# Optimization experiments

Measured on AMD Instinct MI355X. Metric: run time of the kernel, lower is better.

## Reference

```python
import jax, jax.numpy as jnp
import numpy as np

B, L, D_MODEL = 2, 1024, 512
D_INNER, D_STATE, DT_RANK, D_CONV = 1024, 16, 32, 4
N_LAYER, VOCAB, EMBED_DIM, NUM_EMOTIONS = 2, 30000, 256, 7


def setup_inputs() -> dict:
    key = jax.random.key(0)
    ks = jax.random.split(key, 12)
    def n(k, shape, scale=0.02):
        return jax.random.normal(k, shape, jnp.float32) * scale
    A_init = jnp.broadcast_to(jnp.arange(1, D_STATE + 1, dtype=jnp.float32), (N_LAYER, D_INNER, D_STATE))
    return {
        "input_ids": jax.random.randint(ks[0], (B, L), 0, VOCAB),
        "embedding": n(ks[1], (VOCAB, D_MODEL)),
        "norm_w": jnp.ones((N_LAYER, D_MODEL)),
        "in_proj_w": n(ks[2], (N_LAYER, D_MODEL, 2 * D_INNER)),
        "conv_w": n(ks[3], (N_LAYER, D_INNER, 1, D_CONV), 0.1),
        "conv_b": jnp.zeros((N_LAYER, D_INNER)),
        "x_proj_w": n(ks[4], (N_LAYER, D_INNER, DT_RANK + 2 * D_STATE)),
        "dt_proj_w": n(ks[5], (N_LAYER, DT_RANK, D_INNER), 0.1),
        "dt_proj_b": jnp.zeros((N_LAYER, D_INNER)),
        "A_log": jnp.log(A_init),
        "D": jnp.ones((N_LAYER, D_INNER)),
        "out_proj_w": n(ks[6], (N_LAYER, D_INNER, D_MODEL)),
        "norm_f_w": jnp.ones((D_MODEL,)),
        "proj_w": n(ks[7], (D_MODEL, EMBED_DIM)),
        "proj_b": jnp.zeros((EMBED_DIM,)),
        "cls_w": n(ks[8], (EMBED_DIM, NUM_EMOTIONS)),
        "cls_b": jnp.zeros((NUM_EMOTIONS,)),
    }


def rmsnorm(x, w, eps=1e-5):
    return x * jax.lax.rsqrt(jnp.mean(x * x, axis=-1, keepdims=True) + eps) * w


def selective_scan(u, delta, A, B_, C, D_):
    # u, delta: [b,l,d]; A: [d,n]; B_, C: [b,l,n]; D_: [d]
    dA = jnp.exp(jnp.einsum('bld,dn->bldn', delta, A))          # [b,l,d,n]
    dBu = jnp.einsum('bld,bln,bld->bldn', delta, B_, u)          # [b,l,d,n]
    def step(h, inp):
        dA_t, dBu_t, C_t = inp                                   # [b,d,n],[b,d,n],[b,n]
        h = dA_t * h + dBu_t
        y = jnp.einsum('bdn,bn->bd', h, C_t)
        return h, y
    h0 = jnp.zeros((u.shape[0], u.shape[2], A.shape[1]), u.dtype)
    _, ys = jax.lax.scan(step, h0, (dA.transpose(1, 0, 2, 3), dBu.transpose(1, 0, 2, 3), C.transpose(1, 0, 2)))
    return ys.transpose(1, 0, 2) + u * D_                        # [b,l,d]


def mamba_block(x, in_w, cw, cb, xp_w, dt_w, dt_b, A_log, D_, out_w):
    # x: [b,l,d_model]
    xr = x @ in_w                                                # [b,l,2*d_inner]
    xi, res = jnp.split(xr, 2, axis=-1)
    # causal depthwise conv1d over time
    xc = jax.lax.conv_general_dilated(
        xi.transpose(0, 2, 1), cw, window_strides=(1,),
        padding=[(D_CONV - 1, 0)], feature_group_count=D_INNER,
        dimension_numbers=('NCH', 'OIH', 'NCH'))
    xi = jax.nn.silu(xc.transpose(0, 2, 1) + cb)                 # [b,l,d_inner]
    x_dbl = xi @ xp_w
    delta, B_, C = jnp.split(x_dbl, [DT_RANK, DT_RANK + D_STATE], axis=-1)
    delta = jax.nn.softplus(delta @ dt_w + dt_b)                 # [b,l,d_inner]
    A = -jnp.exp(A_log)
    y = selective_scan(xi, delta, A, B_, C, D_)
    y = y * jax.nn.silu(res)
    return y @ out_w                                             # [b,l,d_model]


def reference(input_ids, embedding, norm_w, in_proj_w, conv_w, conv_b, x_proj_w,
              dt_proj_w, dt_proj_b, A_log, D, out_proj_w, norm_f_w,
              proj_w, proj_b, cls_w, cls_b):
    x = embedding[input_ids]                                     # [b,l,d_model]
    for i in range(N_LAYER):
        x = x + mamba_block(rmsnorm(x, norm_w[i]), in_proj_w[i], conv_w[i],
                            conv_b[i], x_proj_w[i], dt_proj_w[i], dt_proj_b[i],
                            A_log[i], D[i], out_proj_w[i])
    x = rmsnorm(x, norm_f_w)
    pooled = x.mean(axis=1)                                      # [b,d_model]
    emotion_emb = pooled @ proj_w + proj_b                       # [b,embed_dim]
    logits = emotion_emb @ cls_w + cls_b                         # [b,num_emotions]
    return logits, emotion_emb
```

## Files before the change

kernel.cpp:

```cpp
#include <hip/hip_runtime.h>
#include <cstddef>

#define D_MODEL   512
#define D_INNER   1024
#define D_STATE   16
#define DT_RANK   32
#define SEQ_L     1024
#define BATCH     2
#define NLAYER    2
#define M_ROWS    (BATCH * SEQ_L)
#define NC        64
#define LC        (SEQ_L / NC)

typedef __bf16 bf16x8 __attribute__((ext_vector_type(8)));
typedef float  f32x4  __attribute__((ext_vector_type(4)));

__device__ __forceinline__ float softplus_f(float x) {
    return fmaxf(x, 0.f) + log1pf(expf(-fabsf(x)));
}
__device__ __forceinline__ float silu_f(float x) {
    return x / (1.f + __expf(-x));
}
__device__ __forceinline__ unsigned short f2bf(float f) {
    unsigned u = __float_as_uint(f);
    return (unsigned short)((u + 0x7fffu + ((u >> 16) & 1u)) >> 16);
}
__device__ __forceinline__ float bf2f(unsigned short v) {
    return __uint_as_float(((unsigned)v) << 16);
}
__device__ __forceinline__ unsigned pack_bf2(float lo, float hi) {
    return (unsigned)f2bf(lo) | ((unsigned)f2bf(hi) << 16);
}

__global__ void embed_kernel(const int* __restrict__ ids,
                             const float* __restrict__ emb,
                             float* __restrict__ x) {
    int g = blockIdx.x * blockDim.x + threadIdx.x;
    int c = (g & 127) << 2;
    int m = g >> 7;
    int row = ids[m];
    *(float4*)&x[(size_t)m * D_MODEL + c] =
        *(const float4*)&emb[(size_t)row * D_MODEL + c];
}

__global__ __launch_bounds__(64) void rmsnorm_bf_kernel(const float* __restrict__ x,
                                                        const float* __restrict__ w,
                                                        unsigned short* __restrict__ out) {
    int row = blockIdx.x;
    int tid = threadIdx.x;
    const float* xp = x + (size_t)row * D_MODEL;
    float4 v0 = *(const float4*)&xp[tid * 4];
    float4 v1 = *(const float4*)&xp[256 + tid * 4];
    float ss = v0.x*v0.x + v0.y*v0.y + v0.z*v0.z + v0.w*v0.w
             + v1.x*v1.x + v1.y*v1.y + v1.z*v1.z + v1.w*v1.w;
    #pragma unroll
    for (int off = 32; off > 0; off >>= 1) ss += __shfl_xor(ss, off);
    float scale = rsqrtf(ss * (1.f / D_MODEL) + 1e-5f);
    float4 w0 = *(const float4*)&w[tid * 4];
    float4 w1 = *(const float4*)&w[256 + tid * 4];
    unsigned short* op = out + (size_t)row * D_MODEL;
    uint2 p0, p1;
    p0.x = pack_bf2(v0.x * scale * w0.x, v0.y * scale * w0.y);
    p0.y = pack_bf2(v0.z * scale * w0.z, v0.w * scale * w0.w);
    p1.x = pack_bf2(v1.x * scale * w1.x, v1.y * scale * w1.y);
    p1.y = pack_bf2(v1.z * scale * w1.z, v1.w * scale * w1.w);
    *(uint2*)&op[tid * 4] = p0;
    *(uint2*)&op[256 + tid * 4] = p1;
}

__global__ __launch_bounds__(256) void castT_kernel(const float* __restrict__ W,
                                                    unsigned short* __restrict__ Wt,
                                                    int K, int N) {
    W  += (size_t)blockIdx.z * K * N;
    Wt += (size_t)blockIdx.z * K * N;
    __shared__ float tile[32][33];
    int n0 = blockIdx.x * 32, k0 = blockIdx.y * 32;
    int tx = threadIdx.x & 31, ty = threadIdx.x >> 5;
    #pragma unroll
    for (int i = 0; i < 4; ++i)
        tile[ty + i*8][tx] = W[(size_t)(k0 + ty + i*8) * N + n0 + tx];
    __syncthreads();
    #pragma unroll
    for (int i = 0; i < 4; ++i)
        Wt[(size_t)(n0 + ty + i*8) * K + k0 + tx] = f2bf(tile[tx][ty + i*8]);
}

__global__ __launch_bounds__(256) void gemm_mfma128(const unsigned short* __restrict__ A,
                                                    const unsigned short* __restrict__ Bt,
                                                    unsigned short* __restrict__ Cb,
                                                    int K, int ldc) {
    __shared__ unsigned short As[128 * 64];
    __shared__ unsigned short Bs[128 * 64];
    int m0 = blockIdx.y * 128;
    int n0 = blockIdx.x * 128;
    int t = threadIdx.x;
    int lane = t & 63, wave = t >> 6;
    int wr = wave >> 1, wc = wave & 1;
    int srow = t >> 3;
    int sc8  = t & 7;
    f32x4 acc[4][4] = {};

    for (int k0 = 0; k0 < K; k0 += 64) {
        __syncthreads();
        #pragma unroll
        for (int i = 0; i < 4; ++i) {
            int row = i * 32 + srow;
            int csrc = sc8 ^ (row & 7);
            __builtin_amdgcn_global_load_lds(
                (const __attribute__((address_space(1))) void*)
                    &A[(size_t)(m0 + row) * K + k0 + csrc * 8],
                (__attribute__((address_space(3))) void*)
                    &As[row * 64 + sc8 * 8], 16, 0, 0);
            __builtin_amdgcn_global_load_lds(
                (const __attribute__((address_space(1))) void*)
                    &Bt[(size_t)(n0 + row) * K + k0 + csrc * 8],
                (__attribute__((address_space(3))) void*)
                    &Bs[row * 64 + sc8 * 8], 16, 0, 0);
        }
        __syncthreads();
        #pragma unroll
        for (int ks = 0; ks < 2; ++ks) {
            bf16x8 av[4], bv[4];
            #pragma unroll
            for (int f = 0; f < 4; ++f) {
                int ar = wr * 64 + f * 16 + (lane & 15);
                int ac = (ks * 4 + (lane >> 4)) ^ (ar & 7);
                av[f] = *reinterpret_cast<const bf16x8*>(&As[ar * 64 + ac * 8]);
                int br = wc * 64 + f * 16 + (lane & 15);
                int bc = (ks * 4 + (lane >> 4)) ^ (br & 7);
                bv[f] = *reinterpret_cast<const bf16x8*>(&Bs[br * 64 + bc * 8]);
            }
            #pragma unroll
            for (int fm = 0; fm < 4; ++fm)
                #pragma unroll
                for (int fn = 0; fn < 4; ++fn)
                    acc[fm][fn] = __builtin_amdgcn_mfma_f32_16x16x32_bf16(
                        av[fm], bv[fn], acc[fm][fn], 0, 0, 0);
        }
    }
    #pragma unroll
    for (int fm = 0; fm < 4; ++fm)
        #pragma unroll
        for (int fn = 0; fn < 4; ++fn) {
            int row = m0 + wr * 64 + fm * 16 + (lane >> 4) * 4;
            int col = n0 + wc * 64 + fn * 16 + (lane & 15);
            #pragma unroll
            for (int r = 0; r < 4; ++r)
                Cb[(size_t)(row + r) * ldc + col] = f2bf(acc[fm][fn][r]);
        }
}

__global__ __launch_bounds__(256) void gemm_mfma64_acc(const unsigned short* __restrict__ A,
                                                       const unsigned short* __restrict__ Bt,
                                                       float* __restrict__ C,
                                                       int K, int ldc) {
    __shared__ unsigned short As[64 * 64];
    __shared__ unsigned short Bs[64 * 64];
    int m0 = blockIdx.y * 64;
    int n0 = blockIdx.x * 64;
    int t = threadIdx.x;
    int lane = t & 63, wave = t >> 6;
    int wr = wave >> 1, wc = wave & 1;
    int srow = t >> 3;
    int sc8  = t & 7;
    f32x4 acc[2][2] = {};

    for (int k0 = 0; k0 < K; k0 += 64) {
        __syncthreads();
        #pragma unroll
        for (int i = 0; i < 2; ++i) {
            int row = i * 32 + srow;
            int csrc = sc8 ^ (row & 7);
            __builtin_amdgcn_global_load_lds(
                (const __attribute__((address_space(1))) void*)
                    &A[(size_t)(m0 + row) * K + k0 + csrc * 8],
                (__attribute__((address_space(3))) void*)
                    &As[row * 64 + sc8 * 8], 16, 0, 0);
            __builtin_amdgcn_global_load_lds(
                (const __attribute__((address_space(1))) void*)
                    &Bt[(size_t)(n0 + row) * K + k0 + csrc * 8],
                (__attribute__((address_space(3))) void*)
                    &Bs[row * 64 + sc8 * 8], 16, 0, 0);
        }
        __syncthreads();
        #pragma unroll
        for (int ks = 0; ks < 2; ++ks) {
            bf16x8 av[2], bv[2];
            #pragma unroll
            for (int f = 0; f < 2; ++f) {
                int ar = wr * 32 + f * 16 + (lane & 15);
                int ac = (ks * 4 + (lane >> 4)) ^ (ar & 7);
                av[f] = *reinterpret_cast<const bf16x8*>(&As[ar * 64 + ac * 8]);
                int br = wc * 32 + f * 16 + (lane & 15);
                int bc = (ks * 4 + (lane >> 4)) ^ (br & 7);
                bv[f] = *reinterpret_cast<const bf16x8*>(&Bs[br * 64 + bc * 8]);
            }
            #pragma unroll
            for (int fm = 0; fm < 2; ++fm)
                #pragma unroll
                for (int fn = 0; fn < 2; ++fn)
                    acc[fm][fn] = __builtin_amdgcn_mfma_f32_16x16x32_bf16(
                        av[fm], bv[fn], acc[fm][fn], 0, 0, 0);
        }
    }
    #pragma unroll
    for (int fm = 0; fm < 2; ++fm)
        #pragma unroll
        for (int fn = 0; fn < 2; ++fn) {
            int row = m0 + wr * 32 + fm * 16 + (lane >> 4) * 4;
            int col = n0 + wc * 32 + fn * 16 + (lane & 15);
            #pragma unroll
            for (int r = 0; r < 4; ++r)
                C[(size_t)(row + r) * ldc + col] += acc[fm][fn][r];
        }
}

__global__ void conv_bf_kernel(const unsigned short* __restrict__ xi,
                               const float* __restrict__ cw,
                               const float* __restrict__ cb,
                               unsigned short* __restrict__ u) {
    int g = blockIdx.x * blockDim.x + threadIdx.x;
    int d = g & (D_INNER - 1);
    int m = g >> 10;
    int l = m & (SEQ_L - 1);
    float4 w = *(const float4*)&cw[d * 4];
    const unsigned short* col = &xi[(size_t)m * 2048 + d];
    float x3 = bf2f(col[0]);
    float x2 = (l >= 1) ? bf2f(col[-2048]) : 0.f;
    float x1 = (l >= 2) ? bf2f(col[-4096]) : 0.f;
    float x0 = (l >= 3) ? bf2f(col[-6144]) : 0.f;
    u[g] = f2bf(silu_f(cb[d] + w.x*x0 + w.y*x1 + w.z*x2 + w.w*x3));
}

__global__ __launch_bounds__(256) void xproj_kernel(const unsigned short* __restrict__ u,
                                                    const float* __restrict__ Bw,
                                                    float* __restrict__ Cc) {
    __shared__ float Bsh[64][68];
    __shared__ float Ash[4][64];
    int row0 = blockIdx.x * 4;
    int t = threadIdx.x;
    int tr = t >> 6, c = t & 63;
    int kk = t >> 2, cb4 = (t & 3) << 4;
    float acc = 0.f;
    for (int k0 = 0; k0 < 1024; k0 += 64) {
        __syncthreads();
        #pragma unroll
        for (int j = 0; j < 4; ++j) {
            float4 v = *(const float4*)&Bw[(size_t)(k0 + kk) * 64 + cb4 + j * 4];
            *(float4*)&Bsh[kk][cb4 + j * 4] = v;
        }
        Ash[tr][c] = bf2f(u[(size_t)(row0 + tr) * 1024 + k0 + c]);
        __syncthreads();
        #pragma unroll
        for (int k = 0; k < 64; ++k)
            acc = fmaf(Ash[tr][k], Bsh[k][c], acc);
    }
    Cc[(size_t)(row0 + tr) * 64 + c] = acc;
}

__global__ __launch_bounds__(256) void scan_p1f(const unsigned short* __restrict__ u,
                                                const float* __restrict__ xdbl,
                                                const float* __restrict__ dtw,
                                                const float* __restrict__ dtb_,
                                                const float* __restrict__ A_log,
                                                float* __restrict__ aprod,
                                                float* __restrict__ hloc) {
    int tid = threadIdx.x;
    int d = blockIdx.x * 256 + tid;
    int b = blockIdx.y, c = blockIdx.z;
    int l0 = c * LC;
    __shared__ float sX[LC][64];
    __shared__ float sW[32][256];
    #pragma unroll
    for (int k = 0; k < 32; ++k)
        sW[k][tid] = dtw[k * 1024 + blockIdx.x * 256 + tid];
    for (int i = tid; i < LC * 64; i += 256) {
        int l = i >> 6, j = i & 63;
        sX[l][j] = xdbl[(size_t)(b * SEQ_L + l0 + l) * 64 + j];
    }
    __syncthreads();
    float A_[D_STATE], h[D_STATE], ap[D_STATE];
    #pragma unroll
    for (int n = 0; n < D_STATE; ++n) {
        A_[n] = -__expf(A_log[(size_t)d * D_STATE + n]);
        h[n] = 0.f; ap[n] = 1.f;
    }
    float dtb = dtb_[d];
    const unsigned short* ucol = u + (size_t)(b * SEQ_L + l0) * D_INNER + d;
    for (int l = 0; l < LC; ++l) {
        float dtv = dtb;
        #pragma unroll
        for (int k = 0; k < 32; ++k) dtv = fmaf(sX[l][k], sW[k][tid], dtv);
        dtv = softplus_f(dtv);
        float uu = bf2f(ucol[l * D_INNER]);
        float du = dtv * uu;
        #pragma unroll
        for (int n = 0; n < D_STATE; ++n) {
            float e = __expf(dtv * A_[n]);
            h[n] = fmaf(e, h[n], du * sX[l][32 + n]);
            ap[n] *= e;
        }
    }
    #pragma unroll
    for (int n = 0; n < D_STATE; ++n) {
        size_t o = (((size_t)b * NC + c) * D_STATE + n) * D_INNER + d;
        aprod[o] = ap[n];
        hloc[o] = h[n];
    }
}

__global__ __launch_bounds__(256) void scan_p2(const float* __restrict__ aprod,
                                               float* __restrict__ hloc) {
    int d = blockIdx.x * 256 + threadIdx.x;
    int n = blockIdx.y;
    int b = blockIdx.z;
    float h = 0.f;
    #pragma unroll 4
    for (int c = 0; c < NC; ++c) {
        size_t o = (((size_t)b * NC + c) * D_STATE + n) * D_INNER + d;
        float ap = aprod[o];
        float lc = hloc[o];
        hloc[o] = h;
        h = fmaf(ap, h, lc);
    }
}

__global__ __launch_bounds__(256) void scan_p3f(const unsigned short* __restrict__ u,
                                                const float* __restrict__ xdbl,
                                                const float* __restrict__ dtw,
                                                const float* __restrict__ dtb_,
                                                const float* __restrict__ A_log,
                                                const float* __restrict__ Dp,
                                                const float* __restrict__ hinit,
                                                const unsigned short* __restrict__ xi,
                                                unsigned short* __restrict__ y) {
    int tid = threadIdx.x;
    int d = blockIdx.x * 256 + tid;
    int b = blockIdx.y, c = blockIdx.z;
    int l0 = c * LC;
    __shared__ float sX[LC][64];
    __shared__ float sW[32][256];
    #pragma unroll
    for (int k = 0; k < 32; ++k)
        sW[k][tid] = dtw[k * 1024 + blockIdx.x * 256 + tid];
    for (int i = tid; i < LC * 64; i += 256) {
        int l = i >> 6, j = i & 63;
        sX[l][j] = xdbl[(size_t)(b * SEQ_L + l0 + l) * 64 + j];
    }
    __syncthreads();
    float A_[D_STATE], h[D_STATE];
    #pragma unroll
    for (int n = 0; n < D_STATE; ++n) {
        A_[n] = -__expf(A_log[(size_t)d * D_STATE + n]);
        size_t o = (((size_t)b * NC + c) * D_STATE + n) * D_INNER + d;
        h[n] = hinit[o];
    }
    float Dd = Dp[d];
    float dtb = dtb_[d];
    const unsigned short* ucol = u  + (size_t)(b * SEQ_L + l0) * D_INNER + d;
    const unsigned short* rcol = xi + (size_t)(b * SEQ_L + l0) * 2048 + 1024 + d;
    for (int l = 0; l < LC; ++l) {
        float dtv = dtb;
        #pragma unroll
        for (int k = 0; k < 32; ++k) dtv = fmaf(sX[l][k], sW[k][tid], dtv);
        dtv = softplus_f(dtv);
        float uu = bf2f(ucol[l * D_INNER]);
        float du = dtv * uu;
        float yv = 0.f;
        #pragma unroll
        for (int n = 0; n < D_STATE; ++n) {
            float e = __expf(dtv * A_[n]);
            h[n] = fmaf(e, h[n], du * sX[l][32 + n]);
            yv = fmaf(h[n], sX[l][48 + n], yv);
        }
        yv = fmaf(uu, Dd, yv);
        float res = bf2f(rcol[l * 2048]);
        y[(size_t)(b * SEQ_L + l0 + l) * D_INNER + d] = f2bf(yv * silu_f(res));
    }
}

__global__ __launch_bounds__(256) void rms_pool1(const float* __restrict__ x,
                                                 float* __restrict__ partial) {
    int blk = blockIdx.x;
    int b = blk >> 5, c = blk & 31;
    int wave = threadIdx.x >> 6, lane = threadIdx.x & 63;
    int row0 = b * SEQ_L + c * 32 + wave * 8;
    float4 a0 = make_float4(0.f, 0.f, 0.f, 0.f);
    float4 a1 = make_float4(0.f, 0.f, 0.f, 0.f);
    for (int r = 0; r < 8; ++r) {
        const float* xp = x + (size_t)(row0 + r) * D_MODEL;
        float4 v0 = *(const float4*)&xp[lane * 4];
        float4 v1 = *(const float4*)&xp[256 + lane * 4];
        float ss = v0.x*v0.x + v0.y*v0.y + v0.z*v0.z + v0.w*v0.w
                 + v1.x*v1.x + v1.y*v1.y + v1.z*v1.z + v1.w*v1.w;
        #pragma unroll
        for (int off = 32; off > 0; off >>= 1) ss += __shfl_xor(ss, off);
        float s = rsqrtf(ss * (1.f / D_MODEL) + 1e-5f);
        a0.x = fmaf(v0.x, s, a0.x); a0.y = fmaf(v0.y, s, a0.y);
        a0.z = fmaf(v0.z, s, a0.z); a0.w = fmaf(v0.w, s, a0.w);
        a1.x = fmaf(v1.x, s, a1.x); a1.y = fmaf(v1.y, s, a1.y);
        a1.z = fmaf(v1.z, s, a1.z); a1.w = fmaf(v1.w, s, a1.w);
    }
    __shared__ float red[4][512];
    *(float4*)&red[wave][lane * 4] = a0;
    *(float4*)&red[wave][256 + lane * 4] = a1;
    __syncthreads();
    int d = threadIdx.x * 2;
    float s0 = red[0][d] + red[1][d] + red[2][d] + red[3][d];
    float s1 = red[0][d+1] + red[1][d+1] + red[2][d+1] + red[3][d+1];
    partial[(size_t)blk * 512 + d]     = s0;
    partial[(size_t)blk * 512 + d + 1] = s1;
}

__global__ __launch_bounds__(256) void embp1f(const float* __restrict__ ppart,
                                              const float* __restrict__ w,
                                              const float* __restrict__ pw,
                                              float* __restrict__ partial) {
    int b = blockIdx.x, kc = blockIdx.y;
    int t = threadIdx.x;
    __shared__ float sp[64];
    if (t < 64) {
        int dd = kc * 64 + t;
        float s = 0.f;
        #pragma unroll
        for (int c = 0; c < 32; ++c)
            s += ppart[((size_t)b * 32 + c) * 512 + dd];
        sp[t] = s * (1.f / SEQ_L) * w[dd];
    }
    __syncthreads();
    float acc = 0.f;
    #pragma unroll 8
    for (int i = 0; i < 64; ++i) {
        int k = kc * 64 + i;
        acc = fmaf(sp[i], pw[(size_t)k * 256 + t], acc);
    }
    partial[((size_t)b * 8 + kc) * 256 + t] = acc;
}

__global__ __launch_bounds__(512) void head_kernel(const float* __restrict__ eparts,
                                                   const float* __restrict__ pb,
                                                   const float* __restrict__ cw,
                                                   const float* __restrict__ cb,
                                                   float* __restrict__ out) {
    __shared__ float se[2][256];
    int t = threadIdx.x;
    int b = t >> 8, e = t & 255;
    float s = pb[e];
    #pragma unroll
    for (int kc = 0; kc < 8; ++kc)
        s += eparts[((size_t)b * 8 + kc) * 256 + e];
    out[14 + b * 256 + e] = s;
    se[b][e] = s;
    __syncthreads();
    int wave = t >> 6, lane = t & 63;
    for (int idx = wave; idx < 14; idx += 8) {
        int bb = idx / 7, cc = idx % 7;
        float a = 0.f;
        #pragma unroll
        for (int i = 0; i < 4; ++i) {
            int k = lane + i * 64;
            a = fmaf(se[bb][k], cw[k * 7 + cc], a);
        }
        #pragma unroll
        for (int off = 32; off > 0; off >>= 1) a += __shfl_xor(a, off);
        if (lane == 0) out[bb * 7 + cc] = a + cb[cc];
    }
}

extern "C" void kernel_launch(void* const* d_in, const int* in_sizes, int n_in,
                              void* d_out, int out_size, void* d_ws, size_t ws_size,
                              hipStream_t stream) {
    const int*   ids    = (const int*)d_in[0];
    const float* emb    = (const float*)d_in[1];
    const float* norm_w = (const float*)d_in[2];
    const float* in_w   = (const float*)d_in[3];
    const float* conv_w = (const float*)d_in[4];
    const float* conv_b = (const float*)d_in[5];
    const float* xp_w   = (const float*)d_in[6];
    const float* dt_w   = (const float*)d_in[7];
    const float* dt_b   = (const float*)d_in[8];
    const float* A_log  = (const float*)d_in[9];
    const float* Dp     = (const float*)d_in[10];
    const float* out_w  = (const float*)d_in[11];
    const float* normf  = (const float*)d_in[12];
    const float* proj_w = (const float*)d_in[13];
    const float* proj_b = (const float*)d_in[14];
    const float* cls_w  = (const float*)d_in[15];
    const float* cls_b  = (const float*)d_in[16];
    float* out = (float*)d_out;

    float* p = (float*)d_ws;
    float* x      = p; p += 1 << 20;
    float* xnr    = p; p += 1 << 20;
    float* xrr    = p; p += 2 << 20;
    float* urr    = p; p += 1 << 20;
    float* xdbl   = p; p += 1 << 17;
    float* wreg   = p; p += 1572864;
    float* aprod  = p; p += 2 << 20;
    float* hloc   = p; p += 2 << 20;
    float* ybr    = p; p += 1 << 20;
    float* eparts = p; p += 4096;

    unsigned short* xn_bf  = (unsigned short*)xnr;
    float*          ppart  = xnr;
    unsigned short* xr_bf  = (unsigned short*)xrr;
    unsigned short* u_bf   = (unsigned short*)urr;
    unsigned short* in_wt_all  = (unsigned short*)wreg;
    unsigned short* out_wt_all = (unsigned short*)(wreg + (1 << 20));
    unsigned short* yb_bf  = (unsigned short*)ybr;

    embed_kernel<<<1024, 256, 0, stream>>>(ids, emb, x);
    castT_kernel<<<dim3(64, 16, NLAYER), 256, 0, stream>>>(in_w, in_wt_all, 512, 2048);
    castT_kernel<<<dim3(16, 32, NLAYER), 256, 0, stream>>>(out_w, out_wt_all, 1024, 512);

    for (int i = 0; i < NLAYER; ++i) {
        unsigned short* in_wt  = in_wt_all  + (size_t)i * 2048 * 512;
        unsigned short* out_wt = out_wt_all + (size_t)i * 512 * 1024;
        const float* dtwi = dt_w + (size_t)i * DT_RANK * D_INNER;
        const float* dtbi = dt_b + (size_t)i * D_INNER;
        const float* Ali  = A_log + (size_t)i * D_INNER * D_STATE;

        rmsnorm_bf_kernel<<<M_ROWS, 64, 0, stream>>>(x, norm_w + i * D_MODEL, xn_bf);
        gemm_mfma128<<<dim3(2048 / 128, M_ROWS / 128), 256, 0, stream>>>(
            xn_bf, in_wt, xr_bf, 512, 2048);
        conv_bf_kernel<<<(M_ROWS * D_INNER) / 256, 256, 0, stream>>>(
            xr_bf, conv_w + (size_t)i * D_INNER * 4, conv_b + (size_t)i * D_INNER, u_bf);
        xproj_kernel<<<M_ROWS / 4, 256, 0, stream>>>(
            u_bf, xp_w + (size_t)i * D_INNER * 64, xdbl);
        scan_p1f<<<dim3(4, BATCH, NC), 256, 0, stream>>>(
            u_bf, xdbl, dtwi, dtbi, Ali, aprod, hloc);
        scan_p2<<<dim3(4, D_STATE, BATCH), 256, 0, stream>>>(aprod, hloc);
        scan_p3f<<<dim3(4, BATCH, NC), 256, 0, stream>>>(
            u_bf, xdbl, dtwi, dtbi, Ali, Dp + (size_t)i * D_INNER, hloc, xr_bf, yb_bf);
        gemm_mfma64_acc<<<dim3(512 / 64, M_ROWS / 64), 256, 0, stream>>>(
            yb_bf, out_wt, x, 1024, 512);
    }

    rms_pool1<<<BATCH * 32, 256, 0, stream>>>(x, ppart);
    embp1f<<<dim3(BATCH, 8), 256, 0, stream>>>(ppart, normf, proj_w, eparts);
    head_kernel<<<1, 512, 0, stream>>>(eparts, proj_b, cls_w, cls_b, out);
}
```

Before: 245.0 us.

## Fuse depthwise conv into xproj and scan kernels, merge init and head launches

Removes the standalone conv kernel and recomputes the causal conv plus SiLU inline in the x-projection and both scan passes, using a rolling register window in the scans. The intermediate u buffer is no longer written and reread. Embedding gather and weight transpose-casts are merged into one launch, and the pooling projection plus classifier head into one single-block kernel. This trades launch count and memory traffic for redundant conv arithmetic and a serial single-block tail.

```diff
diff --git a/kernel.cpp b/kernel.cpp
--- a/kernel.cpp
+++ b/kernel.cpp
@@ -32,15 +32,46 @@
     return (unsigned)f2bf(lo) | ((unsigned)f2bf(hi) << 16);
 }
 
-__global__ void embed_kernel(const int* __restrict__ ids,
-                             const float* __restrict__ emb,
-                             float* __restrict__ x) {
-    int g = blockIdx.x * blockDim.x + threadIdx.x;
-    int c = (g & 127) << 2;
-    int m = g >> 7;
-    int row = ids[m];
-    *(float4*)&x[(size_t)m * D_MODEL + c] =
-        *(const float4*)&emb[(size_t)row * D_MODEL + c];
+__global__ __launch_bounds__(256) void init_kernel(const int* __restrict__ ids,
+                                                   const float* __restrict__ emb,
+                                                   const float* __restrict__ in_w,
+                                                   const float* __restrict__ out_w,
+                                                   float* __restrict__ x,
+                                                   unsigned short* __restrict__ in_wt_all,
+                                                   unsigned short* __restrict__ out_wt_all) {
+    int z = blockIdx.z;
+    if (z == 4) {
+        int blk = blockIdx.y * 64 + blockIdx.x;
+        if (blk >= 1024) return;
+        int g = blk * 256 + threadIdx.x;
+        int c = (g & 127) << 2;
+        int m = g >> 7;
+        int row = ids[m];
+        *(float4*)&x[(size_t)m * D_MODEL + c] =
+            *(const float4*)&emb[(size_t)row * D_MODEL + c];
+        return;
+    }
+    const float* W; unsigned short* Wt; int K, N;
+    if (z < 2) {
+        if (blockIdx.x >= 64 || blockIdx.y >= 16) return;
+        W = in_w + (size_t)z * 512 * 2048; Wt = in_wt_all + (size_t)z * 2048 * 512;
+        K = 512; N = 2048;
+    } else {
+        int zz = z - 2;
+        if (blockIdx.x >= 16 || blockIdx.y >= 32) return;
+        W = out_w + (size_t)zz * 1024 * 512; Wt = out_wt_all + (size_t)zz * 512 * 1024;
+        K = 1024; N = 512;
+    }
+    __shared__ float tile[32][33];
+    int n0 = blockIdx.x * 32, k0 = blockIdx.y * 32;
+    int tx = threadIdx.x & 31, ty = threadIdx.x >> 5;
+    #pragma unroll
+    for (int i = 0; i < 4; ++i)
+        tile[ty + i*8][tx] = W[(size_t)(k0 + ty + i*8) * N + n0 + tx];
+    __syncthreads();
+    #pragma unroll
+    for (int i = 0; i < 4; ++i)
+        Wt[(size_t)(n0 + ty + i*8) * K + k0 + tx] = f2bf(tile[tx][ty + i*8]);
 }
 
 __global__ __launch_bounds__(64) void rmsnorm_bf_kernel(const float* __restrict__ x,
@@ -66,23 +97,6 @@
     p1.y = pack_bf2(v1.z * scale * w1.z, v1.w * scale * w1.w);
     *(uint2*)&op[tid * 4] = p0;
     *(uint2*)&op[256 + tid * 4] = p1;
-}
-
-__global__ __launch_bounds__(256) void castT_kernel(const float* __restrict__ W,
-                                                    unsigned short* __restrict__ Wt,
-                                                    int K, int N) {
-    W  += (size_t)blockIdx.z * K * N;
-    Wt += (size_t)blockIdx.z * K * N;
-    __shared__ float tile[32][33];
-    int n0 = blockIdx.x * 32, k0 = blockIdx.y * 32;
-    int tx = threadIdx.x & 31, ty = threadIdx.x >> 5;
-    #pragma unroll
-    for (int i = 0; i < 4; ++i)
-        tile[ty + i*8][tx] = W[(size_t)(k0 + ty + i*8) * N + n0 + tx];
-    __syncthreads();
-    #pragma unroll
-    for (int i = 0; i < 4; ++i)
-        Wt[(size_t)(n0 + ty + i*8) * K + k0 + tx] = f2bf(tile[tx][ty + i*8]);
 }
 
 __global__ __launch_bounds__(256) void gemm_mfma128(const unsigned short* __restrict__ A,
@@ -215,32 +229,18 @@
         }
 }
 
-__global__ void conv_bf_kernel(const unsigned short* __restrict__ xi,
-                               const float* __restrict__ cw,
-                               const float* __restrict__ cb,
-                               unsigned short* __restrict__ u) {
-    int g = blockIdx.x * blockDim.x + threadIdx.x;
-    int d = g & (D_INNER - 1);
-    int m = g >> 10;
-    int l = m & (SEQ_L - 1);
-    float4 w = *(const float4*)&cw[d * 4];
-    const unsigned short* col = &xi[(size_t)m * 2048 + d];
-    float x3 = bf2f(col[0]);
-    float x2 = (l >= 1) ? bf2f(col[-2048]) : 0.f;
-    float x1 = (l >= 2) ? bf2f(col[-4096]) : 0.f;
-    float x0 = (l >= 3) ? bf2f(col[-6144]) : 0.f;
-    u[g] = f2bf(silu_f(cb[d] + w.x*x0 + w.y*x1 + w.z*x2 + w.w*x3));
-}
-
-__global__ __launch_bounds__(256) void xproj_kernel(const unsigned short* __restrict__ u,
-                                                    const float* __restrict__ Bw,
-                                                    float* __restrict__ Cc) {
+__global__ __launch_bounds__(256) void xproj_f(const unsigned short* __restrict__ xi,
+                                               const float* __restrict__ cw,
+                                               const float* __restrict__ cb,
+                                               const float* __restrict__ Bw,
+                                               float* __restrict__ Cc) {
     __shared__ float Bsh[64][68];
     __shared__ float Ash[4][64];
     int row0 = blockIdx.x * 4;
     int t = threadIdx.x;
     int tr = t >> 6, c = t & 63;
     int kk = t >> 2, cb4 = (t & 3) << 4;
+    int l = (row0 + tr) & (SEQ_L - 1);
     float acc = 0.f;
     for (int k0 = 0; k0 < 1024; k0 += 64) {
         __syncthreads();
@@ -249,7 +249,16 @@
             float4 v = *(const float4*)&Bw[(size_t)(k0 + kk) * 64 + cb4 + j * 4];
             *(float4*)&Bsh[kk][cb4 + j * 4] = v;
         }
-        Ash[tr][c] = bf2f(u[(size_t)(row0 + tr) * 1024 + k0 + c]);
+        {
+            int d = k0 + c;
+            float4 w = *(const float4*)&cw[d * 4];
+            const unsigned short* col = &xi[(size_t)(row0 + tr) * 2048 + d];
+            float x3 = bf2f(col[0]);
+            float x2 = (l >= 1) ? bf2f(col[-2048]) : 0.f;
+            float x1 = (l >= 2) ? bf2f(col[-4096]) : 0.f;
+            float x0 = (l >= 3) ? bf2f(col[-6144]) : 0.f;
+            Ash[tr][c] = silu_f(cb[d] + w.x*x0 + w.y*x1 + w.z*x2 + w.w*x3);
+        }
         __syncthreads();
         #pragma unroll
         for (int k = 0; k < 64; ++k)
@@ -258,10 +267,12 @@
     Cc[(size_t)(row0 + tr) * 64 + c] = acc;
 }
 
-__global__ __launch_bounds__(256) void scan_p1f(const unsigned short* __restrict__ u,
+__global__ __launch_bounds__(256) void scan_p1g(const unsigned short* __restrict__ xi,
                                                 const float* __restrict__ xdbl,
                                                 const float* __restrict__ dtw,
                                                 const float* __restrict__ dtb_,
+                                                const float* __restrict__ cw,
+                                                const float* __restrict__ cb,
                                                 const float* __restrict__ A_log,
                                                 float* __restrict__ aprod,
                                                 float* __restrict__ hloc) {
@@ -285,14 +296,21 @@
         A_[n] = -__expf(A_log[(size_t)d * D_STATE + n]);
         h[n] = 0.f; ap[n] = 1.f;
     }
-    float dtb = dtb_[d];
-    const unsigned short* ucol = u + (size_t)(b * SEQ_L + l0) * D_INNER + d;
+    float4 w = *(const float4*)&cw[d * 4];
+    float cbd = cb[d], dtb = dtb_[d];
+    const unsigned short* xcol = xi + (size_t)(b * SEQ_L + l0) * 2048 + d;
+    float t1 = (l0 >= 1) ? bf2f(xcol[-2048]) : 0.f;
+    float t2 = (l0 >= 2) ? bf2f(xcol[-4096]) : 0.f;
+    float t3 = (l0 >= 3) ? bf2f(xcol[-6144]) : 0.f;
+    #pragma unroll
     for (int l = 0; l < LC; ++l) {
         float dtv = dtb;
         #pragma unroll
         for (int k = 0; k < 32; ++k) dtv = fmaf(sX[l][k], sW[k][tid], dtv);
         dtv = softplus_f(dtv);
-        float uu = bf2f(ucol[l * D_INNER]);
+        float t0 = bf2f(xcol[l * 2048]);
+        float uu = silu_f(cbd + w.x*t3 + w.y*t2 + w.z*t1 + w.w*t0);
+        t3 = t2; t2 = t1; t1 = t0;
         float du = dtv * uu;
         #pragma unroll
         for (int n = 0; n < D_STATE; ++n) {
@@ -325,14 +343,15 @@
     }
 }
 
-__global__ __launch_bounds__(256) void scan_p3f(const unsigned short* __restrict__ u,
+__global__ __launch_bounds__(256) void scan_p3g(const unsigned short* __restrict__ xi,
                                                 const float* __restrict__ xdbl,
                                                 const float* __restrict__ dtw,
                                                 const float* __restrict__ dtb_,
+                                                const float* __restrict__ cw,
+                                                const float* __restrict__ cb,
                                                 const float* __restrict__ A_log,
                                                 const float* __restrict__ Dp,
                                                 const float* __restrict__ hinit,
-                                                const unsigned short* __restrict__ xi,
                                                 unsigned short* __restrict__ y) {
     int tid = threadIdx.x;
     int d = blockIdx.x * 256 + tid;
@@ -356,15 +375,21 @@
         h[n] = hinit[o];
     }
     float Dd = Dp[d];
-    float dtb = dtb_[d];
-    const unsigned short* ucol = u  + (size_t)(b * SEQ_L + l0) * D_INNER + d;
-    const unsigned short* rcol = xi + (size_t)(b * SEQ_L + l0) * 2048 + 1024 + d;
+    float4 w = *(const float4*)&cw[d * 4];
+    float cbd = cb[d], dtb = dtb_[d];
+    const unsigned short* xcol = xi + (size_t)(b * SEQ_L + l0) * 2048 + d;
+    float t1 = (l0 >= 1) ? bf2f(xcol[-2048]) : 0.f;
+    float t2 = (l0 >= 2) ? bf2f(xcol[-4096]) : 0.f;
+    float t3 = (l0 >= 3) ? bf2f(xcol[-6144]) : 0.f;
+    #pragma unroll
     for (int l = 0; l < LC; ++l) {
         float dtv = dtb;
         #pragma unroll
         for (int k = 0; k < 32; ++k) dtv = fmaf(sX[l][k], sW[k][tid], dtv);
         dtv = softplus_f(dtv);
-        float uu = bf2f(ucol[l * D_INNER]);
+        float t0 = bf2f(xcol[l * 2048]);
+        float uu = silu_f(cbd + w.x*t3 + w.y*t2 + w.z*t1 + w.w*t0);
+        t3 = t2; t2 = t1; t1 = t0;
         float du = dtv * uu;
         float yv = 0.f;
         #pragma unroll
@@ -374,7 +399,7 @@
             yv = fmaf(h[n], sX[l][48 + n], yv);
         }
         yv = fmaf(uu, Dd, yv);
-        float res = bf2f(rcol[l * 2048]);
+        float res = bf2f(xcol[l * 2048 + 1024]);
         y[(size_t)(b * SEQ_L + l0 + l) * D_INNER + d] = f2bf(yv * silu_f(res));
     }
 }
@@ -412,58 +437,52 @@
     partial[(size_t)blk * 512 + d + 1] = s1;
 }
 
-__global__ __launch_bounds__(256) void embp1f(const float* __restrict__ ppart,
-                                              const float* __restrict__ w,
-                                              const float* __restrict__ pw,
-                                              float* __restrict__ partial) {
-    int b = blockIdx.x, kc = blockIdx.y;
-    int t = threadIdx.x;
-    __shared__ float sp[64];
-    if (t < 64) {
-        int dd = kc * 64 + t;
-        float s = 0.f;
-        #pragma unroll
-        for (int c = 0; c < 32; ++c)
-            s += ppart[((size_t)b * 32 + c) * 512 + dd];
-        sp[t] = s * (1.f / SEQ_L) * w[dd];
-    }
-    __syncthreads();
-    float acc = 0.f;
-    #pragma unroll 8
-    for (int i = 0; i < 64; ++i) {
-        int k = kc * 64 + i;
-        acc = fmaf(sp[i], pw[(size_t)k * 256 + t], acc);
-    }
-    partial[((size_t)b * 8 + kc) * 256 + t] = acc;
-}
-
-__global__ __launch_bounds__(512) void head_kernel(const float* __restrict__ eparts,
-                                                   const float* __restrict__ pb,
-                                                   const float* __restrict__ cw,
-                                                   const float* __restrict__ cb,
-                                                   float* __restrict__ out) {
+__global__ __launch_bounds__(512) void tail2_kernel(const float* __restrict__ ppart,
+                                                    const float* __restrict__ w,
+                                                    const float* __restrict__ pw,
+                                                    const float* __restrict__ pb,
+                                                    const float* __restrict__ cw,
+                                                    const float* __restrict__ cb,
+                                                    float* __restrict__ out) {
+    __shared__ float sp[2][512];
     __shared__ float se[2][256];
     int t = threadIdx.x;
-    int b = t >> 8, e = t & 255;
-    float s = pb[e];
-    #pragma unroll
-    for (int kc = 0; kc < 8; ++kc)
-        s += eparts[((size_t)b * 8 + kc) * 256 + e];
-    out[14 + b * 256 + e] = s;
-    se[b][e] = s;
+    {
+        int b = t >> 8, dp = (t & 255) * 2;
+        float s0 = 0.f, s1 = 0.f;
+        #pragma unroll 8
+        for (int c = 0; c < 32; ++c) {
+            const float* pp = &ppart[((size_t)b * 32 + c) * 512 + dp];
+            s0 += pp[0]; s1 += pp[1];
+        }
+        sp[b][dp]     = s0 * (1.f / SEQ_L) * w[dp];
+        sp[b][dp + 1] = s1 * (1.f / SEQ_L) * w[dp + 1];
+    }
     __syncthreads();
-    int wave = t >> 6, lane = t & 63;
-    for (int idx = wave; idx < 14; idx += 8) {
-        int bb = idx / 7, cc = idx % 7;
-        float a = 0.f;
-        #pragma unroll
-        for (int i = 0; i < 4; ++i) {
-            int k = lane + i * 64;
-            a = fmaf(se[bb][k], cw[k * 7 + cc], a);
-        }
-        #pragma unroll
-        for (int off = 32; off > 0; off >>= 1) a += __shfl_xor(a, off);
-        if (lane == 0) out[bb * 7 + cc] = a + cb[cc];
+    {
+        int b = t >> 8, e = t & 255;
+        float acc = pb[e];
+        #pragma unroll 8
+        for (int k = 0; k < 512; ++k)
+            acc = fmaf(sp[b][k], pw[(size_t)k * 256 + e], acc);
+        out[14 + b * 256 + e] = acc;
+        se[b][e] = acc;
+    }
+    __syncthreads();
+    {
+        int wave = t >> 6, lane = t & 63;
+        for (int idx = wave; idx < 14; idx += 8) {
+            int bb = idx / 7, cc = idx % 7;
+            float a = 0.f;
+            #pragma unroll
+            for (int i = 0; i < 4; ++i) {
+                int k = lane + i * 64;
+                a = fmaf(se[bb][k], cw[k * 7 + cc], a);
+            }
+            #pragma unroll
+            for (int off = 32; off > 0; off >>= 1) a += __shfl_xor(a, off);
+            if (lane == 0) out[bb * 7 + cc] = a + cb[cc];
+        }
     }
 }
 
@@ -499,44 +518,42 @@
     float* aprod  = p; p += 2 << 20;
     float* hloc   = p; p += 2 << 20;
     float* ybr    = p; p += 1 << 20;
-    float* eparts = p; p += 4096;
+    (void)urr;
 
     unsigned short* xn_bf  = (unsigned short*)xnr;
     float*          ppart  = xnr;
     unsigned short* xr_bf  = (unsigned short*)xrr;
-    unsigned short* u_bf   = (unsigned short*)urr;
     unsigned short* in_wt_all  = (unsigned short*)wreg;
     unsigned short* out_wt_all = (unsigned short*)(wreg + (1 << 20));
     unsigned short* yb_bf  = (unsigned short*)ybr;
 
-    embed_kernel<<<1024, 256, 0, stream>>>(ids, emb, x);
-    castT_kernel<<<dim3(64, 16, NLAYER), 256, 0, stream>>>(in_w, in_wt_all, 512, 2048);
-    castT_kernel<<<dim3(16, 32, NLAYER), 256, 0, stream>>>(out_w, out_wt_all, 1024, 512);
+    init_kernel<<<dim3(64, 32, 5), 256, 0, stream>>>(
+        ids, emb, in_w, out_w, x, in_wt_all, out_wt_all);
 
     for (int i = 0; i < NLAYER; ++i) {
         unsigned short* in_wt  = in_wt_all  + (size_t)i * 2048 * 512;
         unsigned short* out_wt = out_wt_all + (size_t)i * 512 * 1024;
+        const float* cwi  = conv_w + (size_t)i * D_INNER * 4;
+        const float* cbi  = conv_b + (size_t)i * D_INNER;
         const float* dtwi = dt_w + (size_t)i * DT_RANK * D_INNER;
         const float* dtbi = dt_b + (size_t)i * D_INNER;
         const float* Ali  = A_log + (size_t)i * D_INNER * D_STATE;
+        const float* Dpi  = Dp + (size_t)i * D_INNER;
 
         rmsnorm_bf_kernel<<<M_ROWS, 64, 0, stream>>>(x, norm_w + i * D_MODEL, xn_bf);
         gemm_mfma128<<<dim3(2048 / 128, M_ROWS / 128), 256, 0, stream>>>(
             xn_bf, in_wt, xr_bf, 512, 2048);
-        conv_bf_kernel<<<(M_ROWS * D_INNER) / 256, 256, 0, stream>>>(
-            xr_bf, conv_w + (size_t)i * D_INNER * 4, conv_b + (size_t)i * D_INNER, u_bf);
-        xproj_kernel<<<M_ROWS / 4, 256, 0, stream>>>(
-            u_bf, xp_w + (size_t)i * D_INNER * 64, xdbl);
-        scan_p1f<<<dim3(4, BATCH, NC), 256, 0, stream>>>(
-            u_bf, xdbl, dtwi, dtbi, Ali, aprod, hloc);
+        xproj_f<<<M_ROWS / 4, 256, 0, stream>>>(
+            xr_bf, cwi, cbi, xp_w + (size_t)i * D_INNER * 64, xdbl);
+        scan_p1g<<<dim3(4, BATCH, NC), 256, 0, stream>>>(
+            xr_bf, xdbl, dtwi, dtbi, cwi, cbi, Ali, aprod, hloc);
         scan_p2<<<dim3(4, D_STATE, BATCH), 256, 0, stream>>>(aprod, hloc);
-        scan_p3f<<<dim3(4, BATCH, NC), 256, 0, stream>>>(
-            u_bf, xdbl, dtwi, dtbi, Ali, Dp + (size_t)i * D_INNER, hloc, xr_bf, yb_bf);
+        scan_p3g<<<dim3(4, BATCH, NC), 256, 0, stream>>>(
+            xr_bf, xdbl, dtwi, dtbi, cwi, cbi, Ali, Dpi, hloc, yb_bf);
         gemm_mfma64_acc<<<dim3(512 / 64, M_ROWS / 64), 256, 0, stream>>>(
             yb_bf, out_wt, x, 1024, 512);
     }
 
     rms_pool1<<<BATCH * 32, 256, 0, stream>>>(x, ppart);
-    embp1f<<<dim3(BATCH, 8), 256, 0, stream>>>(ppart, normf, proj_w, eparts);
-    head_kernel<<<1, 512, 0, stream>>>(eparts, proj_b, cls_w, cls_b, out);
-}
+    tail2_kernel<<<1, 512, 0, stream>>>(ppart, normf, proj_w, proj_b, cls_w, cls_b, out);
+}
```

Result: slower. 361.2 us (+47.4%).
